# Optimization experiments

Hardware: AMD Instinct MI355X
Metric: run time of the kernel (lower is better)

The kernel has to match this reference:

```python
import jax, jax.numpy as jnp
import numpy as np

N_NODES = 100000
IN_DIM = 128
HID_DIM = 128
N_EDGES = 1600000


def setup_inputs() -> dict:
    key = jax.random.key(0)
    k1, k2, k3, k4 = jax.random.split(key, 4)
    x = jax.random.normal(k1, (N_NODES, IN_DIM), dtype=jnp.float32)
    edge_index = jax.random.randint(k2, (2, N_EDGES), 0, N_NODES, dtype=jnp.int64)
    # GCNConv params (PyG: Linear(in, out, bias=False) + separate bias)
    scale = 1.0 / np.sqrt(IN_DIM)
    weight = jax.random.uniform(k3, (IN_DIM, HID_DIM), jnp.float32, -scale, scale)
    bias = jax.random.uniform(k4, (HID_DIM,), jnp.float32, -scale, scale)
    return {"x": x, "edge_index": edge_index, "weight": weight, "bias": bias}


def _gcn_forward(x, edge_index, weight, bias):
    n = x.shape[0]
    h = x @ weight  # [N, H] linear transform first (PyG order)
    # add self-loops
    loops = jnp.arange(n, dtype=edge_index.dtype)
    src = jnp.concatenate([edge_index[0], loops])
    dst = jnp.concatenate([edge_index[1], loops])
    # symmetric normalization: deg computed on destination (col) per PyG gcn_norm
    ones = jnp.ones_like(dst, dtype=h.dtype)
    deg = jax.ops.segment_sum(ones, dst, num_segments=n)  # [N]
    dinv = jnp.where(deg > 0, jax.lax.rsqrt(deg), 0.0)
    norm = dinv[src] * dinv[dst]  # [E+N]
    # message passing: out[dst] += norm * h[src]
    msg = h[src] * norm[:, None]  # [E+N, H] irregular gather (memory-bound)
    out = jax.ops.segment_sum(msg, dst, num_segments=n)  # scatter-add
    return out + bias


def reference(x, edge_index, weight, bias):
    h = _gcn_forward(x, edge_index, weight, bias)
    return jax.nn.relu(h)  # encoder_type != 'gat' -> ReLU
```

## Files before the change

### kernel.cpp

```cpp
#include <hip/hip_runtime.h>
#include <hip/hip_bf16.h>

#define N_NODES 100000
#define IN_DIM 128
#define HID_DIM 128
#define N_EDGES 1600000
#define NBK 196
#define BCAP 10240
#define BK_EDGES 4096

using short8 = __attribute__((ext_vector_type(8))) short;
using f32x4  = __attribute__((ext_vector_type(4))) float;

__device__ __forceinline__ unsigned short f2bf(float f) {
    unsigned int b = __float_as_uint(f);
    b += 0x7FFFu + ((b >> 16) & 1u);
    return (unsigned short)(b >> 16);
}
__device__ __forceinline__ float bf2f(unsigned short u) {
    return __uint_as_float((unsigned int)u << 16);
}

__global__ void k_prep(const int* __restrict__ ei, int* __restrict__ flag,
                       int* __restrict__ gcur, const float* __restrict__ w,
                       unsigned short* __restrict__ wt) {
    int i = blockIdx.x * 256 + threadIdx.x;
    if (i < NBK) gcur[i] = 0;
    if (i < IN_DIM * HID_DIM) {
        int k = i >> 7, c = i & 127;
        wt[c * 128 + k] = f2bf(w[i]);
    }
    if (blockIdx.x == gridDim.x - 1 && threadIdx.x < 64) {
        int v = ei[2 * threadIdx.x + 1];
        int all0 = __all(v == 0);
        if (threadIdx.x == 0) *flag = all0;
    }
}

__global__ __launch_bounds__(256) void k_binA(const int* __restrict__ ei,
                                              const int* __restrict__ flag,
                                              int* __restrict__ gcur,
                                              uint2* __restrict__ bucket) {
    __shared__ uint2 stage[BK_EDGES];
    __shared__ int hist[NBK], lbase[NBK], lcur[NBK];
    const int tid = threadIdx.x;
    for (int b = tid; b < NBK; b += 256) { hist[b] = 0; lcur[b] = 0; }
    __syncthreads();
    const int is64 = *flag;
    const int e0 = blockIdx.x * BK_EDGES;
    const int valid = min(BK_EDGES, N_EDGES - e0);

#pragma unroll
    for (int k = 0; k < 8; ++k) {
        int el = k * 512 + 2 * tid;
        if (el >= valid) break;
        int e = e0 + el;
        int s0, s1, d0, d1;
        if (is64) {
            int4 vs = reinterpret_cast<const int4*>(ei)[e >> 1];
            int4 vd = (reinterpret_cast<const int4*>(ei) + N_EDGES / 2)[e >> 1];
            s0 = vs.x; s1 = vs.z; d0 = vd.x; d1 = vd.z;
        } else {
            int2 vs = reinterpret_cast<const int2*>(ei)[e >> 1];
            int2 vd = reinterpret_cast<const int2*>(ei + N_EDGES)[e >> 1];
            s0 = vs.x; s1 = vs.y; d0 = vd.x; d1 = vd.y;
        }
        stage[el]     = make_uint2((unsigned)s0, (unsigned)d0);
        stage[el + 1] = make_uint2((unsigned)s1, (unsigned)d1);
        atomicAdd(&hist[d0 >> 9], 1);
        atomicAdd(&hist[d1 >> 9], 1);
    }
    __syncthreads();
    for (int b = tid; b < NBK; b += 256)
        if (hist[b] > 0) lbase[b] = atomicAdd(&gcur[b], hist[b]);
    __syncthreads();
    for (int i = tid; i < valid; i += 256) {
        uint2 v = stage[i];
        int b = v.y >> 9;
        int pos = lbase[b] + atomicAdd(&lcur[b], 1);
        if (pos < BCAP) bucket[(size_t)b * BCAP + pos] = v;
    }
}

__global__ __launch_bounds__(256) void k_buildB(const int* __restrict__ gcur,
                                                const uint2* __restrict__ bucket,
                                                int* __restrict__ cnt,
                                                float* __restrict__ dinv,
                                                int* __restrict__ row_start,
                                                int* __restrict__ csr_src) {
    __shared__ int sizes[NBK];
    __shared__ int ncnt[512], nloff[512], ncur[512];
    __shared__ int base_s, sz_s;
    const int b = blockIdx.x, tid = threadIdx.x;
    for (int i = tid; i < NBK; i += 256) sizes[i] = gcur[i];
    for (int i = tid; i < 512; i += 256) { ncnt[i] = 0; ncur[i] = 0; }
    __syncthreads();
    if (tid == 0) {
        int s = 0;
        for (int i = 0; i < b; ++i) s += sizes[i];
        base_s = s;
        sz_s = min(sizes[b], BCAP);
    }
    __syncthreads();
    const int base = base_s, sz = sz_s;
    const int n0 = b * 512;
    const uint2* bk = bucket + (size_t)b * BCAP;

    for (int i = tid; i < sz; i += 256)
        atomicAdd(&ncnt[bk[i].y - n0], 1);
    __syncthreads();
    if (tid == 0) {
        int s = 0;
        for (int i = 0; i < 512; ++i) { nloff[i] = s; s += ncnt[i]; }
    }
    __syncthreads();
    for (int i = tid; i < 512; i += 256) {
        int node = n0 + i;
        if (node < N_NODES) {
            int c = ncnt[i];
            cnt[node] = c;
            dinv[node] = rsqrtf((float)(c + 1));
            row_start[node] = base + nloff[i];
        }
    }
    for (int i = tid; i < sz; i += 256) {
        uint2 v = bk[i];
        int li = v.y - n0;
        int pos = atomicAdd(&ncur[li], 1);
        csr_src[base + nloff[li] + pos] = (int)v.x;
    }
}

#define LDK 136
__global__ __launch_bounds__(256) void k_gemm(const float* __restrict__ x,
                                              const unsigned short* __restrict__ wt,
                                              unsigned short* __restrict__ h) {
    __shared__ unsigned short xs[64 * LDK];
    __shared__ unsigned short ws[128 * LDK];
    const int tid = threadIdx.x;
    const int brow = blockIdx.x * 64;

    {
        int row = tid >> 2;
        int seg = (tid & 3) * 32;
        int grow = brow + row; if (grow > N_NODES - 1) grow = N_NODES - 1;
        const float4* p = reinterpret_cast<const float4*>(&x[(size_t)grow * IN_DIM + seg]);
#pragma unroll
        for (int i = 0; i < 8; ++i) {
            float4 v = p[i];
            ushort4 u = make_ushort4(f2bf(v.x), f2bf(v.y), f2bf(v.z), f2bf(v.w));
            *reinterpret_cast<ushort4*>(&xs[row * LDK + seg + i * 4]) = u;
        }
    }
    {
        int row = tid >> 1;
        int seg = (tid & 1) * 64;
        const short8* p = reinterpret_cast<const short8*>(&wt[row * 128 + seg]);
#pragma unroll
        for (int i = 0; i < 8; ++i)
            *reinterpret_cast<short8*>(&ws[row * LDK + seg + i * 8]) = p[i];
    }
    __syncthreads();

    const int lane = tid & 63;
    const int wid  = tid >> 6;
    const int m0   = wid * 16;
    const int arow = m0 + (lane & 15);
    const int kgrp = (lane >> 4) * 8;
    f32x4 acc[8] = {};

#pragma unroll
    for (int k0 = 0; k0 < 128; k0 += 32) {
        short8 a = *reinterpret_cast<const short8*>(&xs[arow * LDK + k0 + kgrp]);
#pragma unroll
        for (int nb = 0; nb < 8; ++nb) {
            short8 b = *reinterpret_cast<const short8*>(
                &ws[(nb * 16 + (lane & 15)) * LDK + k0 + kgrp]);
            acc[nb] = __builtin_amdgcn_mfma_f32_16x16x32_bf16(a, b, acc[nb], 0, 0, 0);
        }
    }

#pragma unroll
    for (int nb = 0; nb < 8; ++nb) {
#pragma unroll
        for (int r = 0; r < 4; ++r) {
            int node = brow + m0 + (lane >> 4) * 4 + r;
            int feat = nb * 16 + (lane & 15);
            if (node < N_NODES) h[(size_t)node * HID_DIM + feat] = f2bf(acc[nb][r]);
        }
    }
}

__global__ __launch_bounds__(256) void k_gather(const unsigned short* __restrict__ h,
                                                const int* __restrict__ csr_src,
                                                const int* __restrict__ row_start,
                                                const int* __restrict__ cnt,
                                                const float* __restrict__ dinv,
                                                const float* __restrict__ bias,
                                                float* __restrict__ out) {
    const int lane = threadIdx.x & 63;
    const int l4   = lane & 15;
    const int node = blockIdx.x * 16 + (threadIdx.x >> 6) * 4 + (lane >> 4);
    const int rs = row_start[node];
    const int n  = cnt[node];
    const float di = dinv[node];
    const int tq = n + 1;

    float acc[8] = {};

    for (int c0 = 0; c0 < tq; c0 += 16) {
        int t = c0 + l4;
        int se; float dse;
        if (t < n)       { se = csr_src[rs + t]; dse = dinv[se]; }
        else if (t == n) { se = node; dse = di;   }
        else             { se = node; dse = 0.0f; }
#pragma unroll
        for (int j = 0; j < 16; ++j) {
            int   s  = __shfl(se,  (lane & 48) | j);
            float ds = __shfl(dse, (lane & 48) | j);
            short8 v = *reinterpret_cast<const short8*>(&h[(size_t)s * HID_DIM + l4 * 8]);
#pragma unroll
            for (int b = 0; b < 8; ++b)
                acc[b] = fmaf(ds, bf2f((unsigned short)v[b]), acc[b]);
        }
    }

    float4 bv0 = *reinterpret_cast<const float4*>(&bias[l4 * 8]);
    float4 bv1 = *reinterpret_cast<const float4*>(&bias[l4 * 8 + 4]);
    float4 o0, o1;
    o0.x = fmaxf(fmaf(di, acc[0], bv0.x), 0.0f);
    o0.y = fmaxf(fmaf(di, acc[1], bv0.y), 0.0f);
    o0.z = fmaxf(fmaf(di, acc[2], bv0.z), 0.0f);
    o0.w = fmaxf(fmaf(di, acc[3], bv0.w), 0.0f);
    o1.x = fmaxf(fmaf(di, acc[4], bv1.x), 0.0f);
    o1.y = fmaxf(fmaf(di, acc[5], bv1.y), 0.0f);
    o1.z = fmaxf(fmaf(di, acc[6], bv1.z), 0.0f);
    o1.w = fmaxf(fmaf(di, acc[7], bv1.w), 0.0f);
    *reinterpret_cast<float4*>(&out[(size_t)node * HID_DIM + l4 * 8])     = o0;
    *reinterpret_cast<float4*>(&out[(size_t)node * HID_DIM + l4 * 8 + 4]) = o1;
}

extern "C" void kernel_launch(void* const* d_in, const int* in_sizes, int n_in,
                              void* d_out, int out_size, void* d_ws, size_t ws_size,
                              hipStream_t stream) {
    const float* x    = (const float*)d_in[0];
    const int*   ei   = (const int*)d_in[1];
    const float* w    = (const float*)d_in[2];
    const float* bias = (const float*)d_in[3];
    float* out = (float*)d_out;

    char* wsb = (char*)d_ws;
    unsigned short* h  = (unsigned short*)(wsb);
    int*   cnt       = (int*)(wsb + 25600000);
    float* dinv      = (float*)(wsb + 26000000);
    int*   row_start = (int*)(wsb + 26400000);
    int*   csr_src   = (int*)(wsb + 26800000);
    uint2* bucket    = (uint2*)(wsb + 33200000);
    unsigned short* wt = (unsigned short*)(wsb + 49256320);
    int*   gcur      = (int*)(wsb + 49289088);
    int*   flag      = (int*)(wsb + 49289888);

    k_prep  <<<64, 256, 0, stream>>>(ei, flag, gcur, w, wt);
    k_binA  <<<(N_EDGES + BK_EDGES - 1) / BK_EDGES, 256, 0, stream>>>(ei, flag, gcur, bucket);
    k_buildB<<<NBK, 256, 0, stream>>>(gcur, bucket, cnt, dinv, row_start, csr_src);
    k_gemm  <<<(N_NODES + 63) / 64, 256, 0, stream>>>(x, wt, h);
    k_gather<<<N_NODES / 16, 256, 0, stream>>>(h, csr_src, row_start, cnt, dinv, bias, out);
}
```

Measured before the change: 139.2 us.

## Merge binning and GEMM into one launch, use fp16, parallel scans

Edge binning and the dense GEMM are merged into one kernel whose blocks branch on blockIdx, so the two independent stages run concurrently and one launch is removed. The dtype check moves into each binning block. The intermediate h switches from bf16 to fp16 with native conversions. The serial prefix sums in buildB become wave shuffle scans, and the gather loop is unrolled to process 32 neighbours per iteration with early exits. In exchange, the fat kernel needs more shared memory per block, and fp16 narrows the representable range of h.

New measurement: 125.8 us. -9.6%, faster.

```diff
diff --git a/kernel.cpp b/kernel.cpp
--- a/kernel.cpp
+++ b/kernel.cpp
@@ -8,77 +8,130 @@
 #define NBK 196
 #define BCAP 10240
 #define BK_EDGES 4096
-
-using short8 = __attribute__((ext_vector_type(8))) short;
-using f32x4  = __attribute__((ext_vector_type(4))) float;
-
-__device__ __forceinline__ unsigned short f2bf(float f) {
-    unsigned int b = __float_as_uint(f);
-    b += 0x7FFFu + ((b >> 16) & 1u);
-    return (unsigned short)(b >> 16);
-}
-__device__ __forceinline__ float bf2f(unsigned short u) {
-    return __uint_as_float((unsigned int)u << 16);
-}
-
-__global__ void k_prep(const int* __restrict__ ei, int* __restrict__ flag,
-                       int* __restrict__ gcur, const float* __restrict__ w,
-                       unsigned short* __restrict__ wt) {
+#define NBIN 391
+#define NGEMM 1563
+#define LDK 136
+
+using half8 = __attribute__((ext_vector_type(8))) _Float16;
+using half4 = __attribute__((ext_vector_type(4))) _Float16;
+using f32x4 = __attribute__((ext_vector_type(4))) float;
+
+__global__ void k_prep(int* __restrict__ gcur, const float* __restrict__ w,
+                       _Float16* __restrict__ wt) {
     int i = blockIdx.x * 256 + threadIdx.x;
     if (i < NBK) gcur[i] = 0;
     if (i < IN_DIM * HID_DIM) {
         int k = i >> 7, c = i & 127;
-        wt[c * 128 + k] = f2bf(w[i]);
-    }
-    if (blockIdx.x == gridDim.x - 1 && threadIdx.x < 64) {
-        int v = ei[2 * threadIdx.x + 1];
-        int all0 = __all(v == 0);
-        if (threadIdx.x == 0) *flag = all0;
-    }
-}
-
-__global__ __launch_bounds__(256) void k_binA(const int* __restrict__ ei,
-                                              const int* __restrict__ flag,
+        wt[c * 128 + k] = (_Float16)w[i];
+    }
+}
+
+__global__ __launch_bounds__(256) void k_fat1(const int* __restrict__ ei,
+                                              const float* __restrict__ x,
+                                              const _Float16* __restrict__ wt,
+                                              _Float16* __restrict__ h,
                                               int* __restrict__ gcur,
                                               uint2* __restrict__ bucket) {
-    __shared__ uint2 stage[BK_EDGES];
-    __shared__ int hist[NBK], lbase[NBK], lcur[NBK];
+    __shared__ __align__(16) char smem[52224];
     const int tid = threadIdx.x;
-    for (int b = tid; b < NBK; b += 256) { hist[b] = 0; lcur[b] = 0; }
-    __syncthreads();
-    const int is64 = *flag;
-    const int e0 = blockIdx.x * BK_EDGES;
-    const int valid = min(BK_EDGES, N_EDGES - e0);
-
-#pragma unroll
-    for (int k = 0; k < 8; ++k) {
-        int el = k * 512 + 2 * tid;
-        if (el >= valid) break;
-        int e = e0 + el;
-        int s0, s1, d0, d1;
-        if (is64) {
-            int4 vs = reinterpret_cast<const int4*>(ei)[e >> 1];
-            int4 vd = (reinterpret_cast<const int4*>(ei) + N_EDGES / 2)[e >> 1];
-            s0 = vs.x; s1 = vs.z; d0 = vd.x; d1 = vd.z;
-        } else {
-            int2 vs = reinterpret_cast<const int2*>(ei)[e >> 1];
-            int2 vd = reinterpret_cast<const int2*>(ei + N_EDGES)[e >> 1];
-            s0 = vs.x; s1 = vs.y; d0 = vd.x; d1 = vd.y;
-        }
-        stage[el]     = make_uint2((unsigned)s0, (unsigned)d0);
-        stage[el + 1] = make_uint2((unsigned)s1, (unsigned)d1);
-        atomicAdd(&hist[d0 >> 9], 1);
-        atomicAdd(&hist[d1 >> 9], 1);
-    }
-    __syncthreads();
-    for (int b = tid; b < NBK; b += 256)
-        if (hist[b] > 0) lbase[b] = atomicAdd(&gcur[b], hist[b]);
-    __syncthreads();
-    for (int i = tid; i < valid; i += 256) {
-        uint2 v = stage[i];
-        int b = v.y >> 9;
-        int pos = lbase[b] + atomicAdd(&lcur[b], 1);
-        if (pos < BCAP) bucket[(size_t)b * BCAP + pos] = v;
+
+    if (blockIdx.x < NBIN) {
+        uint2* stage = (uint2*)smem;
+        int* hist  = (int*)(smem + 32768);
+        int* lbase = (int*)(smem + 33552);
+        int* lcur  = (int*)(smem + 34336);
+        int* s64   = (int*)(smem + 35120);
+        for (int b = tid; b < NBK; b += 256) { hist[b] = 0; lcur[b] = 0; }
+        if (tid < 64) {
+            int v = ei[2 * tid + 1];
+            int all0 = __all(v == 0);
+            if (tid == 0) *s64 = all0;
+        }
+        __syncthreads();
+        const int is64 = *s64;
+        const int e0 = blockIdx.x * BK_EDGES;
+        const int valid = min(BK_EDGES, N_EDGES - e0);
+
+#pragma unroll
+        for (int k = 0; k < 8; ++k) {
+            int el = k * 512 + 2 * tid;
+            if (el >= valid) break;
+            int e = e0 + el;
+            int s0, s1, d0, d1;
+            if (is64) {
+                int4 vs = reinterpret_cast<const int4*>(ei)[e >> 1];
+                int4 vd = (reinterpret_cast<const int4*>(ei) + N_EDGES / 2)[e >> 1];
+                s0 = vs.x; s1 = vs.z; d0 = vd.x; d1 = vd.z;
+            } else {
+                int2 vs = reinterpret_cast<const int2*>(ei)[e >> 1];
+                int2 vd = reinterpret_cast<const int2*>(ei + N_EDGES)[e >> 1];
+                s0 = vs.x; s1 = vs.y; d0 = vd.x; d1 = vd.y;
+            }
+            stage[el]     = make_uint2((unsigned)s0, (unsigned)d0);
+            stage[el + 1] = make_uint2((unsigned)s1, (unsigned)d1);
+            atomicAdd(&hist[d0 >> 9], 1);
+            atomicAdd(&hist[d1 >> 9], 1);
+        }
+        __syncthreads();
+        for (int b = tid; b < NBK; b += 256)
+            if (hist[b] > 0) lbase[b] = atomicAdd(&gcur[b], hist[b]);
+        __syncthreads();
+        for (int i = tid; i < valid; i += 256) {
+            uint2 v = stage[i];
+            int b = v.y >> 9;
+            int pos = lbase[b] + atomicAdd(&lcur[b], 1);
+            if (pos < BCAP) bucket[(size_t)b * BCAP + pos] = v;
+        }
+    } else {
+        _Float16* xs = (_Float16*)smem;
+        _Float16* ws = (_Float16*)(smem + 17408);
+        const int brow = (blockIdx.x - NBIN) * 64;
+        {
+            int row = tid >> 2;
+            int seg = (tid & 3) * 32;
+            int grow = brow + row; if (grow > N_NODES - 1) grow = N_NODES - 1;
+            const float4* p = reinterpret_cast<const float4*>(&x[(size_t)grow * IN_DIM + seg]);
+#pragma unroll
+            for (int i = 0; i < 8; ++i) {
+                float4 v = p[i];
+                half4 hv = {(_Float16)v.x, (_Float16)v.y, (_Float16)v.z, (_Float16)v.w};
+                *reinterpret_cast<half4*>(&xs[row * LDK + seg + i * 4]) = hv;
+            }
+        }
+        {
+            int row = tid >> 1;
+            int seg = (tid & 1) * 64;
+            const half8* p = reinterpret_cast<const half8*>(&wt[row * 128 + seg]);
+#pragma unroll
+            for (int i = 0; i < 8; ++i)
+                *reinterpret_cast<half8*>(&ws[row * LDK + seg + i * 8]) = p[i];
+        }
+        __syncthreads();
+
+        const int lane = tid & 63;
+        const int m0   = (tid >> 6) * 16;
+        const int arow = m0 + (lane & 15);
+        const int kgrp = (lane >> 4) * 8;
+        f32x4 acc[8] = {};
+#pragma unroll
+        for (int k0 = 0; k0 < 128; k0 += 32) {
+            half8 a = *reinterpret_cast<const half8*>(&xs[arow * LDK + k0 + kgrp]);
+#pragma unroll
+            for (int nb = 0; nb < 8; ++nb) {
+                half8 b = *reinterpret_cast<const half8*>(
+                    &ws[(nb * 16 + (lane & 15)) * LDK + k0 + kgrp]);
+                acc[nb] = __builtin_amdgcn_mfma_f32_16x16x32_f16(a, b, acc[nb], 0, 0, 0);
+            }
+        }
+#pragma unroll
+        for (int nb = 0; nb < 8; ++nb) {
+#pragma unroll
+            for (int r = 0; r < 4; ++r) {
+                int node = brow + m0 + (lane >> 4) * 4 + r;
+                int feat = nb * 16 + (lane & 15);
+                if (node < N_NODES) h[(size_t)node * HID_DIM + feat] = (_Float16)acc[nb][r];
+            }
+        }
     }
 }
 
@@ -90,30 +143,42 @@
                                                 int* __restrict__ csr_src) {
     __shared__ int sizes[NBK];
     __shared__ int ncnt[512], nloff[512], ncur[512];
-    __shared__ int base_s, sz_s;
+    __shared__ int wtot[4];
+    __shared__ int base_s;
     const int b = blockIdx.x, tid = threadIdx.x;
     for (int i = tid; i < NBK; i += 256) sizes[i] = gcur[i];
-    for (int i = tid; i < 512; i += 256) { ncnt[i] = 0; ncur[i] = 0; }
-    __syncthreads();
-    if (tid == 0) {
-        int s = 0;
-        for (int i = 0; i < b; ++i) s += sizes[i];
-        base_s = s;
-        sz_s = min(sizes[b], BCAP);
-    }
-    __syncthreads();
-    const int base = base_s, sz = sz_s;
+    ncnt[tid] = 0; ncnt[tid + 256] = 0; ncur[tid] = 0; ncur[tid + 256] = 0;
+    __syncthreads();
+    const int sz = min(sizes[b], BCAP);
+    if (tid < 64) {
+        int part = 0;
+        for (int i = tid; i < b; i += 64) part += sizes[i];
+#pragma unroll
+        for (int d = 32; d; d >>= 1) part += __shfl_xor(part, d);
+        if (tid == 0) base_s = part;
+    }
     const int n0 = b * 512;
     const uint2* bk = bucket + (size_t)b * BCAP;
-
-    for (int i = tid; i < sz; i += 256)
-        atomicAdd(&ncnt[bk[i].y - n0], 1);
-    __syncthreads();
-    if (tid == 0) {
-        int s = 0;
-        for (int i = 0; i < 512; ++i) { nloff[i] = s; s += ncnt[i]; }
-    }
-    __syncthreads();
+    for (int i = tid; i < sz; i += 256) atomicAdd(&ncnt[bk[i].y - n0], 1);
+    __syncthreads();
+    int c0 = ncnt[2 * tid], c1 = ncnt[2 * tid + 1];
+    int pair = c0 + c1;
+    int lane = tid & 63, wv = tid >> 6;
+    int scan = pair;
+#pragma unroll
+    for (int d = 1; d < 64; d <<= 1) {
+        int t = __shfl_up(scan, d);
+        if (lane >= d) scan += t;
+    }
+    if (lane == 63) wtot[wv] = scan;
+    int excl = scan - pair;
+    __syncthreads();
+#pragma unroll
+    for (int i = 0; i < 4; ++i) if (i < wv) excl += wtot[i];
+    nloff[2 * tid] = excl;
+    nloff[2 * tid + 1] = excl + c0;
+    __syncthreads();
+    const int base = base_s;
     for (int i = tid; i < 512; i += 256) {
         int node = n0 + i;
         if (node < N_NODES) {
@@ -131,67 +196,24 @@
     }
 }
 
-#define LDK 136
-__global__ __launch_bounds__(256) void k_gemm(const float* __restrict__ x,
-                                              const unsigned short* __restrict__ wt,
-                                              unsigned short* __restrict__ h) {
-    __shared__ unsigned short xs[64 * LDK];
-    __shared__ unsigned short ws[128 * LDK];
-    const int tid = threadIdx.x;
-    const int brow = blockIdx.x * 64;
-
-    {
-        int row = tid >> 2;
-        int seg = (tid & 3) * 32;
-        int grow = brow + row; if (grow > N_NODES - 1) grow = N_NODES - 1;
-        const float4* p = reinterpret_cast<const float4*>(&x[(size_t)grow * IN_DIM + seg]);
-#pragma unroll
-        for (int i = 0; i < 8; ++i) {
-            float4 v = p[i];
-            ushort4 u = make_ushort4(f2bf(v.x), f2bf(v.y), f2bf(v.z), f2bf(v.w));
-            *reinterpret_cast<ushort4*>(&xs[row * LDK + seg + i * 4]) = u;
-        }
-    }
-    {
-        int row = tid >> 1;
-        int seg = (tid & 1) * 64;
-        const short8* p = reinterpret_cast<const short8*>(&wt[row * 128 + seg]);
-#pragma unroll
-        for (int i = 0; i < 8; ++i)
-            *reinterpret_cast<short8*>(&ws[row * LDK + seg + i * 8]) = p[i];
-    }
-    __syncthreads();
-
-    const int lane = tid & 63;
-    const int wid  = tid >> 6;
-    const int m0   = wid * 16;
-    const int arow = m0 + (lane & 15);
-    const int kgrp = (lane >> 4) * 8;
-    f32x4 acc[8] = {};
-
-#pragma unroll
-    for (int k0 = 0; k0 < 128; k0 += 32) {
-        short8 a = *reinterpret_cast<const short8*>(&xs[arow * LDK + k0 + kgrp]);
-#pragma unroll
-        for (int nb = 0; nb < 8; ++nb) {
-            short8 b = *reinterpret_cast<const short8*>(
-                &ws[(nb * 16 + (lane & 15)) * LDK + k0 + kgrp]);
-            acc[nb] = __builtin_amdgcn_mfma_f32_16x16x32_bf16(a, b, acc[nb], 0, 0, 0);
-        }
-    }
-
-#pragma unroll
-    for (int nb = 0; nb < 8; ++nb) {
-#pragma unroll
-        for (int r = 0; r < 4; ++r) {
-            int node = brow + m0 + (lane >> 4) * 4 + r;
-            int feat = nb * 16 + (lane & 15);
-            if (node < N_NODES) h[(size_t)node * HID_DIM + feat] = f2bf(acc[nb][r]);
-        }
-    }
-}
-
-__global__ __launch_bounds__(256) void k_gather(const unsigned short* __restrict__ h,
+#define GSTEP(J, SE, DS) {                                                   \
+    int s_ = __shfl(SE, hi | (J));                                           \
+    float w_ = __shfl(DS, hi | (J));                                         \
+    half8 v_ = *reinterpret_cast<const half8*>(hbase + (size_t)s_ * HID_DIM);\
+    acc[0] = fmaf((float)v_[0], w_, acc[0]);                                 \
+    acc[1] = fmaf((float)v_[1], w_, acc[1]);                                 \
+    acc[2] = fmaf((float)v_[2], w_, acc[2]);                                 \
+    acc[3] = fmaf((float)v_[3], w_, acc[3]);                                 \
+    acc[4] = fmaf((float)v_[4], w_, acc[4]);                                 \
+    acc[5] = fmaf((float)v_[5], w_, acc[5]);                                 \
+    acc[6] = fmaf((float)v_[6], w_, acc[6]);                                 \
+    acc[7] = fmaf((float)v_[7], w_, acc[7]); }
+#define GGRP(B, SE, DS) \
+    GSTEP(B + 0, SE, DS) GSTEP(B + 1, SE, DS) GSTEP(B + 2, SE, DS) \
+    GSTEP(B + 3, SE, DS) GSTEP(B + 4, SE, DS) GSTEP(B + 5, SE, DS) \
+    GSTEP(B + 6, SE, DS) GSTEP(B + 7, SE, DS)
+
+__global__ __launch_bounds__(256) void k_gather(const _Float16* __restrict__ h,
                                                 const int* __restrict__ csr_src,
                                                 const int* __restrict__ row_start,
                                                 const int* __restrict__ cnt,
@@ -200,29 +222,32 @@
                                                 float* __restrict__ out) {
     const int lane = threadIdx.x & 63;
     const int l4   = lane & 15;
+    const int hi   = lane & 48;
     const int node = blockIdx.x * 16 + (threadIdx.x >> 6) * 4 + (lane >> 4);
     const int rs = row_start[node];
     const int n  = cnt[node];
     const float di = dinv[node];
     const int tq = n + 1;
+    const _Float16* hbase = h + l4 * 8;
 
     float acc[8] = {};
 
-    for (int c0 = 0; c0 < tq; c0 += 16) {
-        int t = c0 + l4;
-        int se; float dse;
-        if (t < n)       { se = csr_src[rs + t]; dse = dinv[se]; }
-        else if (t == n) { se = node; dse = di;   }
-        else             { se = node; dse = 0.0f; }
-#pragma unroll
-        for (int j = 0; j < 16; ++j) {
-            int   s  = __shfl(se,  (lane & 48) | j);
-            float ds = __shfl(dse, (lane & 48) | j);
-            short8 v = *reinterpret_cast<const short8*>(&h[(size_t)s * HID_DIM + l4 * 8]);
-#pragma unroll
-            for (int b = 0; b < 8; ++b)
-                acc[b] = fmaf(ds, bf2f((unsigned short)v[b]), acc[b]);
-        }
+    for (int c0 = 0; c0 < tq; c0 += 32) {
+        int t0 = c0 + l4, t1 = t0 + 16;
+        int se0 = node, se1 = node;
+        float dw0 = 0.0f, dw1 = 0.0f;
+        if (t0 < n)       { se0 = csr_src[rs + t0]; dw0 = dinv[se0]; }
+        else if (t0 == n)   dw0 = di;
+        if (t1 < n)       { se1 = csr_src[rs + t1]; dw1 = dinv[se1]; }
+        else if (t1 == n)   dw1 = di;
+
+        GGRP(0, se0, dw0)
+        if (tq <= c0 + 8) continue;
+        GGRP(8, se0, dw0)
+        if (tq <= c0 + 16) continue;
+        GGRP(0, se1, dw1)
+        if (tq <= c0 + 24) continue;
+        GGRP(8, se1, dw1)
     }
 
     float4 bv0 = *reinterpret_cast<const float4*>(&bias[l4 * 8]);
@@ -250,19 +275,17 @@
     float* out = (float*)d_out;
 
     char* wsb = (char*)d_ws;
-    unsigned short* h  = (unsigned short*)(wsb);
+    _Float16* h      = (_Float16*)(wsb);
     int*   cnt       = (int*)(wsb + 25600000);
     float* dinv      = (float*)(wsb + 26000000);
     int*   row_start = (int*)(wsb + 26400000);
     int*   csr_src   = (int*)(wsb + 26800000);
     uint2* bucket    = (uint2*)(wsb + 33200000);
-    unsigned short* wt = (unsigned short*)(wsb + 49256320);
+    _Float16* wt     = (_Float16*)(wsb + 49256320);
     int*   gcur      = (int*)(wsb + 49289088);
-    int*   flag      = (int*)(wsb + 49289888);
-
-    k_prep  <<<64, 256, 0, stream>>>(ei, flag, gcur, w, wt);
-    k_binA  <<<(N_EDGES + BK_EDGES - 1) / BK_EDGES, 256, 0, stream>>>(ei, flag, gcur, bucket);
+
+    k_prep  <<<64, 256, 0, stream>>>(gcur, w, wt);
+    k_fat1  <<<NBIN + NGEMM, 256, 0, stream>>>(ei, x, wt, h, gcur, bucket);
     k_buildB<<<NBK, 256, 0, stream>>>(gcur, bucket, cnt, dinv, row_start, csr_src);
-    k_gemm  <<<(N_NODES + 63) / 64, 256, 0, stream>>>(x, wt, h);
     k_gather<<<N_NODES / 16, 256, 0, stream>>>(h, csr_src, row_start, cnt, dinv, bias, out);
 }
```
